# Performance work log

Hardware: AMD Instinct MI355X
Metric: run time of the kernel (lower is better)

Reference implementation:

```python
import jax, jax.numpy as jnp
import numpy as np

V, E, T, H, L, FF = 32000, 512, 2048, 8, 6, 2048
B = 2
HD = E // H
EPS = 1e-5


def setup_inputs() -> dict:
    key = jax.random.key(0)
    ks = iter(jax.random.split(key, 32))
    s = 0.02
    d = {
        "x": jax.random.randint(next(ks), (B, T), 0, V),
        "tok_emb": jax.random.normal(next(ks), (V, E), jnp.float32) * s,
        "pos_emb": jax.random.normal(next(ks), (T, E), jnp.float32) * s,
        "Wq": jax.random.normal(next(ks), (L, E, E), jnp.float32) * s,
        "bq": jnp.zeros((L, E), jnp.float32),
        "Wk": jax.random.normal(next(ks), (L, E, E), jnp.float32) * s,
        "bk": jnp.zeros((L, E), jnp.float32),
        "Wv": jax.random.normal(next(ks), (L, E, E), jnp.float32) * s,
        "bv": jnp.zeros((L, E), jnp.float32),
        "Wo": jax.random.normal(next(ks), (L, E, E), jnp.float32) * s,
        "bo": jnp.zeros((L, E), jnp.float32),
        "ln1_s": jnp.ones((L, E), jnp.float32),
        "ln1_b": jnp.zeros((L, E), jnp.float32),
        "ln2_s": jnp.ones((L, E), jnp.float32),
        "ln2_b": jnp.zeros((L, E), jnp.float32),
        "W1": jax.random.normal(next(ks), (L, E, FF), jnp.float32) * s,
        "b1": jnp.zeros((L, FF), jnp.float32),
        "W2": jax.random.normal(next(ks), (L, FF, E), jnp.float32) * s,
        "b2": jnp.zeros((L, E), jnp.float32),
        "Wout": jax.random.normal(next(ks), (E, V), jnp.float32) * s,
        "bout": jnp.zeros((V,), jnp.float32),
    }
    return d


def _layernorm(x, scale, bias):
    mu = jnp.mean(x, axis=-1, keepdims=True)
    var = jnp.var(x, axis=-1, keepdims=True)
    return (x - mu) * jax.lax.rsqrt(var + EPS) * scale + bias


def reference(x, tok_emb, pos_emb, Wq, bq, Wk, bk, Wv, bv, Wo, bo,
              ln1_s, ln1_b, ln2_s, ln2_b, W1, b1, W2, b2, Wout, bout):
    b, t = x.shape
    h = tok_emb[x] + pos_emb[:t][None]  # [b,t,E]
    causal = jnp.tril(jnp.ones((t, t), bool))  # True on/below diag
    for i in range(L):
        y = _layernorm(h, ln1_s[i], ln1_b[i])
        q = (y @ Wq[i] + bq[i]).reshape(b, t, H, HD)
        k = (y @ Wk[i] + bk[i]).reshape(b, t, H, HD)
        v = (y @ Wv[i] + bv[i]).reshape(b, t, H, HD)
        scores = jnp.einsum("bqhd,bkhd->bhqk", q, k) / np.sqrt(HD).astype(np.float32)
        scores = jnp.where(causal, scores, -jnp.inf)
        attn = jax.nn.softmax(scores, axis=-1)
        o = jnp.einsum("bhqk,bkhd->bqhd", attn, v).reshape(b, t, E)
        h = h + (o @ Wo[i] + bo[i])  # dropout is identity at eval
        y = _layernorm(h, ln2_s[i], ln2_b[i])
        ff = jax.nn.relu(y @ W1[i] + b1[i]) @ W2[i] + b2[i]
        h = h + ff
    return h @ Wout + bout  # [b,t,V]
```

## Files before the change

kernel.cpp:

```cpp
#include <hip/hip_runtime.h>
#include <cstdint>
#include <cstddef>

#define TOKENS 4096
#define E_ 512
#define T_ 2048
#define H_ 8
#define L_ 6
#define FF_ 2048
#define V_ 32000

typedef unsigned short u16;
typedef __attribute__((ext_vector_type(8))) short short8;
typedef __attribute__((ext_vector_type(4))) float f32x4;

__device__ __forceinline__ u16 f2b(float f) {
  union { float f; unsigned u; } x; x.f = f;
  unsigned r = x.u + 0x7fffu + ((x.u >> 16) & 1u);
  return (u16)(r >> 16);
}

__device__ __forceinline__ void gload_lds16(const void* g, void* l) {
  __builtin_amdgcn_global_load_lds((__attribute__((address_space(1))) void*)(uintptr_t)g,
                                   (__attribute__((address_space(3))) void*)l, 16, 0, 0);
}

template<int BF16OUT, int RESID, int RELU>
__global__ __launch_bounds__(256) void gemm_bt(
    const u16* __restrict__ A, const u16* __restrict__ BT,
    const float* __restrict__ bias, const float* __restrict__ resid,
    void* __restrict__ outp, int M, int N, int K, int ldc)
{
  __shared__ u16 a_sm[2][128 * 32];
  __shared__ u16 b_sm[2][128 * 32];
  const int tid  = threadIdx.x;
  const int wave = tid >> 6;
  const int lane = tid & 63;
  const int l16  = lane & 15;
  const int quad = lane >> 4;
  const int bm = blockIdx.y << 7;
  const int bn = blockIdx.x << 7;
  const int wr = (wave >> 1) << 6;
  const int wc = (wave & 1) << 6;

  const int srow = tid >> 2;
  const int soff = (tid & 3) << 3;
  const u16* ag0 = A  + (size_t)(bm + srow) * K + soff;
  const u16* ag1 = A  + (size_t)(bm + 64 + srow) * K + soff;
  const u16* bg0 = BT + (size_t)(bn + srow) * K + soff;
  const u16* bg1 = BT + (size_t)(bn + 64 + srow) * K + soff;

  auto stage = [&](int buf, int k0) {
    gload_lds16(ag0 + k0, a_sm[buf] + wave * 512);
    gload_lds16(ag1 + k0, a_sm[buf] + 2048 + wave * 512);
    gload_lds16(bg0 + k0, b_sm[buf] + wave * 512);
    gload_lds16(bg1 + k0, b_sm[buf] + 2048 + wave * 512);
  };

  f32x4 acc[4][4] = {};
  const int ksteps = K >> 5;
  stage(0, 0);
  int cur = 0;
  for (int t = 0; t < ksteps; ++t) {
    __syncthreads();
    if (t + 1 < ksteps) stage(cur ^ 1, (t + 1) << 5);
    short8 af[4], bf[4];
#pragma unroll
    for (int mt = 0; mt < 4; ++mt)
      af[mt] = *(const short8*)&a_sm[cur][(wr + mt * 16 + l16) * 32 + quad * 8];
#pragma unroll
    for (int nt = 0; nt < 4; ++nt)
      bf[nt] = *(const short8*)&b_sm[cur][(wc + nt * 16 + l16) * 32 + quad * 8];
#pragma unroll
    for (int mt = 0; mt < 4; ++mt)
#pragma unroll
      for (int nt = 0; nt < 4; ++nt)
        acc[mt][nt] = __builtin_amdgcn_mfma_f32_16x16x32_bf16(af[mt], bf[nt], acc[mt][nt], 0, 0, 0);
    cur ^= 1;
  }

#pragma unroll
  for (int mt = 0; mt < 4; ++mt) {
#pragma unroll
    for (int nt = 0; nt < 4; ++nt) {
      const int cg = bn + wc + nt * 16 + l16;
      const int rg = bm + wr + mt * 16 + quad * 4;
      const float bv = bias[cg];
#pragma unroll
      for (int i = 0; i < 4; ++i) {
        float v = acc[mt][nt][i] + bv;
        size_t idx = (size_t)(rg + i) * ldc + cg;
        if (RESID) v += resid[idx];
        if (RELU)  v = fmaxf(v, 0.f);
        if (BF16OUT) ((u16*)outp)[idx] = f2b(v);
        else         ((float*)outp)[idx] = v;
      }
    }
  }
}

template<int BF16OUT, int RELU>
__global__ __launch_bounds__(256) void gemm_bt64(
    const u16* __restrict__ A, const u16* __restrict__ BT,
    const float* __restrict__ bias, void* __restrict__ outp,
    int M, int N, int K, int ldc)
{
  __shared__ u16 a_sm[2][64 * 32];
  __shared__ u16 b_sm[2][128 * 32];
  const int tid  = threadIdx.x;
  const int wave = tid >> 6;
  const int lane = tid & 63;
  const int l16  = lane & 15;
  const int quad = lane >> 4;
  const int bm = blockIdx.y << 6;
  const int bn = blockIdx.x << 7;
  const int wr = (wave >> 1) << 5;
  const int wc = (wave & 1) << 6;

  const int srow = tid >> 2;
  const int soff = (tid & 3) << 3;
  const u16* ag  = A  + (size_t)(bm + srow) * K + soff;
  const u16* bg0 = BT + (size_t)(bn + srow) * K + soff;
  const u16* bg1 = BT + (size_t)(bn + 64 + srow) * K + soff;

  auto stage = [&](int buf, int k0) {
    gload_lds16(ag  + k0, a_sm[buf] + wave * 512);
    gload_lds16(bg0 + k0, b_sm[buf] + wave * 512);
    gload_lds16(bg1 + k0, b_sm[buf] + 2048 + wave * 512);
  };

  f32x4 acc[2][4] = {};
  const int ksteps = K >> 5;
  stage(0, 0);
  int cur = 0;
  for (int t = 0; t < ksteps; ++t) {
    __syncthreads();
    if (t + 1 < ksteps) stage(cur ^ 1, (t + 1) << 5);
    short8 af[2], bf[4];
#pragma unroll
    for (int mt = 0; mt < 2; ++mt)
      af[mt] = *(const short8*)&a_sm[cur][(wr + mt * 16 + l16) * 32 + quad * 8];
#pragma unroll
    for (int nt = 0; nt < 4; ++nt)
      bf[nt] = *(const short8*)&b_sm[cur][(wc + nt * 16 + l16) * 32 + quad * 8];
#pragma unroll
    for (int mt = 0; mt < 2; ++mt)
#pragma unroll
      for (int nt = 0; nt < 4; ++nt)
        acc[mt][nt] = __builtin_amdgcn_mfma_f32_16x16x32_bf16(af[mt], bf[nt], acc[mt][nt], 0, 0, 0);
    cur ^= 1;
  }

#pragma unroll
  for (int mt = 0; mt < 2; ++mt) {
#pragma unroll
    for (int nt = 0; nt < 4; ++nt) {
      const int cg = bn + wc + nt * 16 + l16;
      const int rg = bm + wr + mt * 16 + quad * 4;
      const float bv = bias[cg];
#pragma unroll
      for (int i = 0; i < 4; ++i) {
        float v = acc[mt][nt][i] + bv;
        size_t idx = (size_t)(rg + i) * ldc + cg;
        if (RELU)  v = fmaxf(v, 0.f);
        if (BF16OUT) ((u16*)outp)[idx] = f2b(v);
        else         ((float*)outp)[idx] = v;
      }
    }
  }
}

__global__ __launch_bounds__(256) void gemm_sk64(
    const u16* __restrict__ A, const u16* __restrict__ BT,
    float* __restrict__ part, int M, int N, int lda, int kLen)
{
  __shared__ u16 a_sm[2][64 * 32];
  __shared__ u16 b_sm[2][128 * 32];
  const int tid  = threadIdx.x;
  const int wave = tid >> 6;
  const int lane = tid & 63;
  const int l16  = lane & 15;
  const int quad = lane >> 4;
  const int bm = blockIdx.y << 6;
  const int bn = blockIdx.x << 7;
  const int wr = (wave >> 1) << 5;
  const int wc = (wave & 1) << 6;

  const u16* Ab = A  + (size_t)blockIdx.z * kLen;
  const u16* Bb = BT + (size_t)blockIdx.z * kLen;

  const int srow = tid >> 2;
  const int soff = (tid & 3) << 3;
  const u16* ag  = Ab + (size_t)(bm + srow) * lda + soff;
  const u16* bg0 = Bb + (size_t)(bn + srow) * lda + soff;
  const u16* bg1 = Bb + (size_t)(bn + 64 + srow) * lda + soff;

  auto stage = [&](int buf, int k0) {
    gload_lds16(ag  + k0, a_sm[buf] + wave * 512);
    gload_lds16(bg0 + k0, b_sm[buf] + wave * 512);
    gload_lds16(bg1 + k0, b_sm[buf] + 2048 + wave * 512);
  };

  f32x4 acc[2][4] = {};
  const int ksteps = kLen >> 5;
  stage(0, 0);
  int cur = 0;
  for (int t = 0; t < ksteps; ++t) {
    __syncthreads();
    if (t + 1 < ksteps) stage(cur ^ 1, (t + 1) << 5);
    short8 af[2], bf[4];
#pragma unroll
    for (int mt = 0; mt < 2; ++mt)
      af[mt] = *(const short8*)&a_sm[cur][(wr + mt * 16 + l16) * 32 + quad * 8];
#pragma unroll
    for (int nt = 0; nt < 4; ++nt)
      bf[nt] = *(const short8*)&b_sm[cur][(wc + nt * 16 + l16) * 32 + quad * 8];
#pragma unroll
    for (int mt = 0; mt < 2; ++mt)
#pragma unroll
      for (int nt = 0; nt < 4; ++nt)
        acc[mt][nt] = __builtin_amdgcn_mfma_f32_16x16x32_bf16(af[mt], bf[nt], acc[mt][nt], 0, 0, 0);
    cur ^= 1;
  }

  float* out = part + (size_t)blockIdx.z * M * N;
#pragma unroll
  for (int mt = 0; mt < 2; ++mt) {
#pragma unroll
    for (int nt = 0; nt < 4; ++nt) {
      const int cg = bn + wc + nt * 16 + l16;
      const int rg = bm + wr + mt * 16 + quad * 4;
#pragma unroll
      for (int i = 0; i < 4; ++i)
        out[(size_t)(rg + i) * N + cg] = acc[mt][nt][i];
    }
  }
}

__global__ __launch_bounds__(256) void attn_kernel(const u16* __restrict__ qkv,
                                                   u16* __restrict__ o)
{
  __shared__ u16 k_sm[2][64 * 64];
  __shared__ u16 vT_sm[2][64 * 64];
  __shared__ u16 p_sm[4 * 16 * 64];
  const int tid  = threadIdx.x;
  const int wave = tid >> 6;
  const int lane = tid & 63;
  const int l16  = lane & 15;
  const int quad = lane >> 4;
  const int j  = blockIdx.x;
  const int bh = blockIdx.y;
  const int b  = bh >> 3, h = bh & 7;
  const size_t base = (size_t)b * T_ * 1536;

  const int qrow = j * 64 + wave * 16 + l16;
  short8 aq[2];
#pragma unroll
  for (int half = 0; half < 2; ++half)
    aq[half] = *(const short8*)&qkv[base + (size_t)qrow * 1536 + h * 64 + half * 32 + quad * 8];

  f32x4 oacc[4] = {};
  float m_i[4] = {-INFINITY, -INFINITY, -INFINITY, -INFINITY};
  float l_i[4] = {0.f, 0.f, 0.f, 0.f};

  const int ksrc = ((tid & 7) ^ ((tid >> 3) & 7)) * 8;
  auto stageK = [&](int kt, int buf) {
    gload_lds16(qkv + base + (size_t)(kt * 64 + (tid >> 3)) * 1536 + 512 + h * 64 + ksrc,
                k_sm[buf] + wave * 512);
    gload_lds16(qkv + base + (size_t)(kt * 64 + 32 + (tid >> 3)) * 1536 + 512 + h * 64 + ksrc,
                k_sm[buf] + 2048 + wave * 512);
  };
  const int vt = tid >> 2, vd0 = (tid & 3) * 16;
  auto loadV = [&](int kt, short8* vr) {
    const u16* vp = &qkv[base + (size_t)(kt * 64 + vt) * 1536 + 1024 + h * 64 + vd0];
    vr[0] = *(const short8*)vp;
    vr[1] = *(const short8*)(vp + 8);
  };
  auto writeV = [&](int buf, const short8* vr) {
#pragma unroll
    for (int i = 0; i < 8; ++i) vT_sm[buf][(vd0 + i) * 64 + (vt ^ (i << 3))] = (u16)vr[0][i];
#pragma unroll
    for (int i = 0; i < 8; ++i) vT_sm[buf][(vd0 + 8 + i) * 64 + (vt ^ (i << 3))] = (u16)vr[1][i];
  };

  const int nkt = j + 1;
  short8 vr[2], vrn[2];
  stageK(0, 0);
  loadV(0, vr);
  writeV(0, vr);
  int cur = 0;
  for (int kt = 0; kt < nkt; ++kt) {
    __syncthreads();
    if (kt + 1 < nkt) { stageK(kt + 1, cur ^ 1); loadV(kt + 1, vrn); }

    f32x4 s[4] = {};
#pragma unroll
    for (int nt = 0; nt < 4; ++nt)
#pragma unroll
      for (int half = 0; half < 2; ++half) {
        short8 bk = *(const short8*)&k_sm[cur][(nt * 16 + l16) * 64 +
                                              (((half * 4 + quad) ^ (l16 & 7)) << 3)];
        s[nt] = __builtin_amdgcn_mfma_f32_16x16x32_bf16(aq[half], bk, s[nt], 0, 0, 0);
      }
#pragma unroll
    for (int nt = 0; nt < 4; ++nt)
#pragma unroll
      for (int i = 0; i < 4; ++i) {
        const int col = kt * 64 + nt * 16 + l16;
        const int row = j * 64 + wave * 16 + quad * 4 + i;
        float sv = s[nt][i] * 0.125f;
        s[nt][i] = (col <= row) ? sv : -INFINITY;
      }
    float rm[4], mn[4], alpha[4], rs[4], p[4][4];
#pragma unroll
    for (int i = 0; i < 4; ++i)
      rm[i] = fmaxf(fmaxf(s[0][i], s[1][i]), fmaxf(s[2][i], s[3][i]));
#pragma unroll
    for (int off = 1; off < 16; off <<= 1)
#pragma unroll
      for (int i = 0; i < 4; ++i) rm[i] = fmaxf(rm[i], __shfl_xor(rm[i], off));
#pragma unroll
    for (int i = 0; i < 4; ++i) {
      mn[i] = fmaxf(m_i[i], rm[i]);
      alpha[i] = __expf(m_i[i] - mn[i]);
      m_i[i] = mn[i];
#pragma unroll
      for (int nt = 0; nt < 4; ++nt) p[nt][i] = __expf(s[nt][i] - mn[i]);
      rs[i] = (p[0][i] + p[1][i]) + (p[2][i] + p[3][i]);
    }
#pragma unroll
    for (int off = 1; off < 16; off <<= 1)
#pragma unroll
      for (int i = 0; i < 4; ++i) rs[i] += __shfl_xor(rs[i], off);
#pragma unroll
    for (int i = 0; i < 4; ++i) l_i[i] = l_i[i] * alpha[i] + rs[i];
#pragma unroll
    for (int nt = 0; nt < 4; ++nt)
#pragma unroll
      for (int i = 0; i < 4; ++i) oacc[nt][i] *= alpha[i];
    u16* pw = p_sm + wave * 1024;
#pragma unroll
    for (int i = 0; i < 4; ++i) {
      const int pr = quad * 4 + i;
#pragma unroll
      for (int nt = 0; nt < 4; ++nt)
        pw[pr * 64 + ((nt * 16 + l16) ^ ((pr & 7) << 3))] = f2b(p[nt][i]);
    }
    asm volatile("s_waitcnt lgkmcnt(0)" ::: "memory");
    short8 pf[2];
#pragma unroll
    for (int kh = 0; kh < 2; ++kh)
      pf[kh] = *(const short8*)&pw[l16 * 64 + (((kh * 4 + quad) ^ (l16 & 7)) << 3)];
#pragma unroll
    for (int nt = 0; nt < 4; ++nt)
#pragma unroll
      for (int kh = 0; kh < 2; ++kh) {
        short8 bv = *(const short8*)&vT_sm[cur][(nt * 16 + l16) * 64 +
                                               (((kh * 4 + quad) ^ (l16 & 7)) << 3)];
        oacc[nt] = __builtin_amdgcn_mfma_f32_16x16x32_bf16(pf[kh], bv, oacc[nt], 0, 0, 0);
      }

    if (kt + 1 < nkt) writeV(cur ^ 1, vrn);
    cur ^= 1;
  }
#pragma unroll
  for (int nt = 0; nt < 4; ++nt)
#pragma unroll
    for (int i = 0; i < 4; ++i) {
      const int row = j * 64 + wave * 16 + quad * 4 + i;
      const float ov = oacc[nt][i] / l_i[i];
      o[(size_t)(b * T_ + row) * 512 + h * 64 + nt * 16 + l16] = f2b(ov);
    }
}

__device__ __forceinline__ void ln_emit(float2 hv, const float* __restrict__ sc,
                                        const float* __restrict__ bi, int tid,
                                        unsigned* __restrict__ yrow)
{
  float s = hv.x + hv.y;
  float q = hv.x * hv.x + hv.y * hv.y;
  for (int off = 32; off; off >>= 1) { s += __shfl_down(s, off); q += __shfl_down(q, off); }
  __shared__ float red[8];
  const int wave = tid >> 6, lane = tid & 63;
  if (!lane) { red[wave] = s; red[4 + wave] = q; }
  __syncthreads();
  if (tid == 0) {
    float ts = 0, tq = 0;
    for (int w = 0; w < 4; ++w) { ts += red[w]; tq += red[4 + w]; }
    red[0] = ts; red[4] = tq;
  }
  __syncthreads();
  const float mu = red[0] * (1.f / 512.f);
  const float var = red[4] * (1.f / 512.f) - mu * mu;
  const float rstd = rsqrtf(var + 1e-5f);
  const float y0 = (hv.x - mu) * rstd * sc[tid * 2]     + bi[tid * 2];
  const float y1 = (hv.y - mu) * rstd * sc[tid * 2 + 1] + bi[tid * 2 + 1];
  yrow[tid] = ((unsigned)f2b(y1) << 16) | (unsigned)f2b(y0);
}

template<int NS, int DOLN>
__global__ __launch_bounds__(256) void resid_ln_kernel(
    const float* __restrict__ part, const float* __restrict__ bias,
    float* __restrict__ h, const float* __restrict__ sc,
    const float* __restrict__ bi, u16* __restrict__ y)
{
  const int row = blockIdx.x, tid = threadIdx.x;
  float2 hv = ((const float2*)(h + (size_t)row * 512))[tid];
  const float2 bv = ((const float2*)bias)[tid];
#pragma unroll
  for (int s = 0; s < NS; ++s) {
    const float2 pv = ((const float2*)(part + ((size_t)s * TOKENS + row) * 512))[tid];
    hv.x += pv.x; hv.y += pv.y;
  }
  hv.x += bv.x; hv.y += bv.y;
  ((float2*)(h + (size_t)row * 512))[tid] = hv;
  if (DOLN)
    ln_emit(hv, sc, bi, tid, (unsigned*)(y + (size_t)row * 512));
  else
    ((unsigned*)y)[(size_t)row * 256 + tid] = ((unsigned)f2b(hv.y) << 16) | (unsigned)f2b(hv.x);
}

__global__ __launch_bounds__(256) void embed_ln_kernel(const int* __restrict__ x,
                                                       const float* __restrict__ tok,
                                                       const float* __restrict__ pos,
                                                       const float* __restrict__ sc,
                                                       const float* __restrict__ bi,
                                                       float* __restrict__ h,
                                                       u16* __restrict__ y)
{
  const int row = blockIdx.x, tid = threadIdx.x;
  const int t = row & (T_ - 1);
  const int tk = x[row];
  const float2 a = ((const float2*)tok)[(size_t)tk * 256 + tid];
  const float2 p = ((const float2*)pos)[(size_t)t * 256 + tid];
  float2 hv = make_float2(a.x + p.x, a.y + p.y);
  ((float2*)(h + (size_t)row * 512))[tid] = hv;
  ln_emit(hv, sc, bi, tid, (unsigned*)(y + (size_t)row * 512));
}

__global__ void transW(const float* __restrict__ src, u16* __restrict__ dst,
                       int K, int N, long sStr, long dStr)
{
  __shared__ float tile[32][33];
  const int l = blockIdx.z;
  const float* S = src + (size_t)l * sStr;
  u16* D = dst + (size_t)l * dStr;
  const int n0 = blockIdx.x * 32, k0 = blockIdx.y * 32;
  const int tx = threadIdx.x, ty = threadIdx.y;
#pragma unroll
  for (int i = 0; i < 4; ++i)
    tile[ty + 8 * i][tx] = S[(size_t)(k0 + ty + 8 * i) * N + n0 + tx];
  __syncthreads();
#pragma unroll
  for (int i = 0; i < 4; ++i)
    D[(size_t)(n0 + ty + 8 * i) * K + k0 + tx] = f2b(tile[tx][ty + 8 * i]);
}

__global__ __launch_bounds__(256) void bias_cat_kernel(const float* __restrict__ bq,
                                                       const float* __restrict__ bk,
                                                       const float* __restrict__ bv,
                                                       float* __restrict__ o)
{
  const int i = blockIdx.x * 256 + threadIdx.x;
  if (i >= L_ * 1536) return;
  const int l = i / 1536, c = i % 1536;
  float v = (c < 512) ? bq[l * 512 + c] : (c < 1024) ? bk[l * 512 + c - 512] : bv[l * 512 + c - 1024];
  o[i] = v;
}

extern "C" void kernel_launch(void* const* d_in, const int* in_sizes, int n_in,
                              void* d_out, int out_size, void* d_ws, size_t ws_size,
                              hipStream_t stream) {
  const int*   x     = (const int*)d_in[0];
  const float* tok   = (const float*)d_in[1];
  const float* pos   = (const float*)d_in[2];
  const float* Wq    = (const float*)d_in[3];
  const float* bq    = (const float*)d_in[4];
  const float* Wk    = (const float*)d_in[5];
  const float* bk    = (const float*)d_in[6];
  const float* Wv    = (const float*)d_in[7];
  const float* bv    = (const float*)d_in[8];
  const float* Wo    = (const float*)d_in[9];
  const float* bo    = (const float*)d_in[10];
  const float* ln1s  = (const float*)d_in[11];
  const float* ln1b  = (const float*)d_in[12];
  const float* ln2s  = (const float*)d_in[13];
  const float* ln2b  = (const float*)d_in[14];
  const float* W1    = (const float*)d_in[15];
  const float* b1    = (const float*)d_in[16];
  const float* W2    = (const float*)d_in[17];
  const float* b2    = (const float*)d_in[18];
  const float* Wout  = (const float*)d_in[19];
  const float* bout  = (const float*)d_in[20];

  char* ws = (char*)d_ws;
  size_t off = 0;
  auto alloc = [&](size_t bytes) { char* p = ws + off; off += (bytes + 255) & ~(size_t)255; return p; };
  u16*   qkvT  = (u16*)alloc((size_t)L_ * 1536 * 512 * 2);
  u16*   WoT   = (u16*)alloc((size_t)L_ * 512 * 512 * 2);
  u16*   W1T   = (u16*)alloc((size_t)L_ * 2048 * 512 * 2);
  u16*   W2T   = (u16*)alloc((size_t)L_ * 512 * 2048 * 2);
  u16*   WoutT = (u16*)alloc((size_t)V_ * 512 * 2);
  float* bqkv  = (float*)alloc((size_t)L_ * 1536 * 4);
  float* h     = (float*)alloc((size_t)TOKENS * 512 * 4);
  u16*   y     = (u16*)alloc((size_t)TOKENS * 512 * 2);
  u16*   qkv   = (u16*)alloc((size_t)TOKENS * 1536 * 2);
  u16*   obuf  = (u16*)alloc((size_t)TOKENS * 512 * 2);
  u16*   ff    = (u16*)alloc((size_t)TOKENS * 2048 * 2);
  u16*   hb    = (u16*)alloc((size_t)TOKENS * 512 * 2);
  float* part  = (float*)alloc((size_t)4 * TOKENS * 512 * 4);
  (void)ws_size; (void)in_sizes; (void)n_in; (void)out_size;

  transW<<<dim3(16, 16, L_), dim3(32, 8), 0, stream>>>(Wq, qkvT,             512, 512, 512L * 512, 1536L * 512);
  transW<<<dim3(16, 16, L_), dim3(32, 8), 0, stream>>>(Wk, qkvT + 512 * 512, 512, 512, 512L * 512, 1536L * 512);
  transW<<<dim3(16, 16, L_), dim3(32, 8), 0, stream>>>(Wv, qkvT + 1024 * 512,512, 512, 512L * 512, 1536L * 512);
  transW<<<dim3(16, 16, L_), dim3(32, 8), 0, stream>>>(Wo, WoT,              512, 512, 512L * 512, 512L * 512);
  transW<<<dim3(64, 16, L_), dim3(32, 8), 0, stream>>>(W1, W1T,  512, 2048, 512L * 2048, 2048L * 512);
  transW<<<dim3(16, 64, L_), dim3(32, 8), 0, stream>>>(W2, W2T, 2048,  512, 2048L * 512, 512L * 2048);
  transW<<<dim3(1000, 16, 1), dim3(32, 8), 0, stream>>>(Wout, WoutT, 512, V_, 0, 0);
  bias_cat_kernel<<<36, 256, 0, stream>>>(bq, bk, bv, bqkv);

  embed_ln_kernel<<<TOKENS, 256, 0, stream>>>(x, tok, pos, ln1s, ln1b, h, y);

  for (int l = 0; l < L_; ++l) {
    gemm_bt64<1, 0><<<dim3(12, 64), 256, 0, stream>>>(
        y, qkvT + (size_t)l * 1536 * 512, bqkv + l * 1536, qkv, TOKENS, 1536, 512, 1536);
    attn_kernel<<<dim3(32, 16), 256, 0, stream>>>(qkv, obuf);
    gemm_sk64<<<dim3(4, 64, 2), 256, 0, stream>>>(
        obuf, WoT + (size_t)l * 512 * 512, part, TOKENS, 512, 512, 256);
    resid_ln_kernel<2, 1><<<TOKENS, 256, 0, stream>>>(
        part, bo + l * 512, h, ln2s + l * 512, ln2b + l * 512, y);
    gemm_bt64<1, 1><<<dim3(16, 64), 256, 0, stream>>>(
        y, W1T + (size_t)l * 2048 * 512, b1 + l * 2048, ff, TOKENS, 2048, 512, 2048);
    gemm_sk64<<<dim3(4, 64, 2), 256, 0, stream>>>(
        ff, W2T + (size_t)l * 512 * 2048, part, TOKENS, 512, 2048, 1024);
    if (l < L_ - 1)
      resid_ln_kernel<2, 1><<<TOKENS, 256, 0, stream>>>(
          part, b2 + l * 512, h, ln1s + (l + 1) * 512, ln1b + (l + 1) * 512, y);
    else
      resid_ln_kernel<2, 0><<<TOKENS, 256, 0, stream>>>(
          part, b2 + l * 512, h, nullptr, nullptr, hb);
  }

  gemm_bt<0, 0, 0><<<dim3(250, 32), 256, 0, stream>>>(
      hb, WoutT, bout, nullptr, (float*)d_out, TOKENS, V_, 512, V_);
}
```

Before: 1.833 ms.

## Merge weight-transpose launches, fold bias concat into embed, swizzle and stream logits GEMM

All weight transposes now run in one launch that picks its matrix from the block index, and the QKV bias concat moves into the embedding kernel, removing eight small launches. The vocabulary GEMM remaps block indices across eight groups to change which tiles run together, and writes its fp32 logits with nontemporal stores so they bypass the cache. Attention reverses the query-tile order for the second batch, which is meant to spread causal work more evenly. The split-K partial buffer is shrunk to the two slices actually used, and the unused residual path is removed.

```diff
diff --git a/kernel.cpp b/kernel.cpp
--- a/kernel.cpp
+++ b/kernel.cpp
@@ -25,11 +25,11 @@
                                    (__attribute__((address_space(3))) void*)l, 16, 0, 0);
 }
 
-template<int BF16OUT, int RESID, int RELU>
+template<int BF16OUT, int RELU>
 __global__ __launch_bounds__(256) void gemm_bt(
     const u16* __restrict__ A, const u16* __restrict__ BT,
-    const float* __restrict__ bias, const float* __restrict__ resid,
-    void* __restrict__ outp, int M, int N, int K, int ldc)
+    const float* __restrict__ bias, void* __restrict__ outp,
+    int M, int N, int K, int ldc)
 {
   __shared__ u16 a_sm[2][128 * 32];
   __shared__ u16 b_sm[2][128 * 32];
@@ -38,8 +38,11 @@
   const int lane = tid & 63;
   const int l16  = lane & 15;
   const int quad = lane >> 4;
-  const int bm = blockIdx.y << 7;
-  const int bn = blockIdx.x << 7;
+  int id = blockIdx.y * gridDim.x + blockIdx.x;
+  const int cpx = (gridDim.x * gridDim.y) >> 3;
+  id = (id & 7) * cpx + (id >> 3);
+  const int bm = (id / gridDim.x) << 7;
+  const int bn = (id % gridDim.x) << 7;
   const int wr = (wave >> 1) << 6;
   const int wc = (wave & 1) << 6;
 
@@ -90,10 +93,9 @@
       for (int i = 0; i < 4; ++i) {
         float v = acc[mt][nt][i] + bv;
         size_t idx = (size_t)(rg + i) * ldc + cg;
-        if (RESID) v += resid[idx];
         if (RELU)  v = fmaxf(v, 0.f);
         if (BF16OUT) ((u16*)outp)[idx] = f2b(v);
-        else         ((float*)outp)[idx] = v;
+        else         __builtin_nontemporal_store(v, (float*)outp + idx);
       }
     }
   }
@@ -248,8 +250,8 @@
   const int lane = tid & 63;
   const int l16  = lane & 15;
   const int quad = lane >> 4;
-  const int j  = blockIdx.x;
   const int bh = blockIdx.y;
+  const int j  = (bh < 8) ? blockIdx.x : 31 - blockIdx.x;
   const int b  = bh >> 3, h = bh & 7;
   const size_t base = (size_t)b * T_ * 1536;
 
@@ -425,10 +427,22 @@
                                                        const float* __restrict__ pos,
                                                        const float* __restrict__ sc,
                                                        const float* __restrict__ bi,
+                                                       const float* __restrict__ bq,
+                                                       const float* __restrict__ bk,
+                                                       const float* __restrict__ bv,
+                                                       float* __restrict__ bqkv,
                                                        float* __restrict__ h,
                                                        u16* __restrict__ y)
 {
   const int row = blockIdx.x, tid = threadIdx.x;
+  if (row < 36) {
+    const int i = row * 256 + tid;
+    if (i < L_ * 1536) {
+      const int l = i / 1536, c = i % 1536;
+      bqkv[i] = (c < 512) ? bq[l * 512 + c]
+              : (c < 1024) ? bk[l * 512 + c - 512] : bv[l * 512 + c - 1024];
+    }
+  }
   const int t = row & (T_ - 1);
   const int tk = x[row];
   const float2 a = ((const float2*)tok)[(size_t)tk * 256 + tid];
@@ -438,14 +452,42 @@
   ln_emit(hv, sc, bi, tid, (unsigned*)(y + (size_t)row * 512));
 }
 
-__global__ void transW(const float* __restrict__ src, u16* __restrict__ dst,
-                       int K, int N, long sStr, long dStr)
+__global__ void transW_all(const float* __restrict__ Wq, const float* __restrict__ Wk,
+                           const float* __restrict__ Wv, const float* __restrict__ Wo,
+                           const float* __restrict__ W1, const float* __restrict__ W2,
+                           const float* __restrict__ Wout,
+                           u16* __restrict__ qkvT, u16* __restrict__ WoT,
+                           u16* __restrict__ W1T, u16* __restrict__ W2T,
+                           u16* __restrict__ WoutT)
 {
   __shared__ float tile[32][33];
-  const int l = blockIdx.z;
-  const float* S = src + (size_t)l * sStr;
-  u16* D = dst + (size_t)l * dStr;
-  const int n0 = blockIdx.x * 32, k0 = blockIdx.y * 32;
+  int f = blockIdx.x;
+  const float* S; u16* D; int N, Kd, n0, k0;
+  if (f < 16000) {
+    S = Wout; D = WoutT; N = 32000; Kd = 512;
+    n0 = (f % 1000) * 32; k0 = (f / 1000) * 32;
+  } else {
+    f -= 16000;
+    const int l = f / 3072, r = f % 3072;
+    if (r < 1024) {
+      const int w = r >> 8, rr = r & 255;
+      S = (w == 0 ? Wq : w == 1 ? Wk : w == 2 ? Wv : Wo) + (size_t)l * 512 * 512;
+      D = (w < 3) ? qkvT + (size_t)l * 1536 * 512 + (size_t)w * 512 * 512
+                  : WoT + (size_t)l * 512 * 512;
+      N = 512; Kd = 512;
+      n0 = (rr & 15) * 32; k0 = (rr >> 4) * 32;
+    } else if (r < 2048) {
+      const int rr = r - 1024;
+      S = W1 + (size_t)l * 512 * 2048; D = W1T + (size_t)l * 2048 * 512;
+      N = 2048; Kd = 512;
+      n0 = (rr & 63) * 32; k0 = (rr >> 6) * 32;
+    } else {
+      const int rr = r - 2048;
+      S = W2 + (size_t)l * 2048 * 512; D = W2T + (size_t)l * 512 * 2048;
+      N = 512; Kd = 2048;
+      n0 = (rr & 15) * 32; k0 = (rr >> 4) * 32;
+    }
+  }
   const int tx = threadIdx.x, ty = threadIdx.y;
 #pragma unroll
   for (int i = 0; i < 4; ++i)
@@ -453,19 +495,7 @@
   __syncthreads();
 #pragma unroll
   for (int i = 0; i < 4; ++i)
-    D[(size_t)(n0 + ty + 8 * i) * K + k0 + tx] = f2b(tile[tx][ty + 8 * i]);
-}
-
-__global__ __launch_bounds__(256) void bias_cat_kernel(const float* __restrict__ bq,
-                                                       const float* __restrict__ bk,
-                                                       const float* __restrict__ bv,
-                                                       float* __restrict__ o)
-{
-  const int i = blockIdx.x * 256 + threadIdx.x;
-  if (i >= L_ * 1536) return;
-  const int l = i / 1536, c = i % 1536;
-  float v = (c < 512) ? bq[l * 512 + c] : (c < 1024) ? bk[l * 512 + c - 512] : bv[l * 512 + c - 1024];
-  o[i] = v;
+    D[(size_t)(n0 + ty + 8 * i) * Kd + k0 + tx] = f2b(tile[tx][ty + 8 * i]);
 }
 
 extern "C" void kernel_launch(void* const* d_in, const int* in_sizes, int n_in,
@@ -508,19 +538,14 @@
   u16*   obuf  = (u16*)alloc((size_t)TOKENS * 512 * 2);
   u16*   ff    = (u16*)alloc((size_t)TOKENS * 2048 * 2);
   u16*   hb    = (u16*)alloc((size_t)TOKENS * 512 * 2);
-  float* part  = (float*)alloc((size_t)4 * TOKENS * 512 * 4);
+  float* part  = (float*)alloc((size_t)2 * TOKENS * 512 * 4);
   (void)ws_size; (void)in_sizes; (void)n_in; (void)out_size;
 
-  transW<<<dim3(16, 16, L_), dim3(32, 8), 0, stream>>>(Wq, qkvT,             512, 512, 512L * 512, 1536L * 512);
-  transW<<<dim3(16, 16, L_), dim3(32, 8), 0, stream>>>(Wk, qkvT + 512 * 512, 512, 512, 512L * 512, 1536L * 512);
-  transW<<<dim3(16, 16, L_), dim3(32, 8), 0, stream>>>(Wv, qkvT + 1024 * 512,512, 512, 512L * 512, 1536L * 512);
-  transW<<<dim3(16, 16, L_), dim3(32, 8), 0, stream>>>(Wo, WoT,              512, 512, 512L * 512, 512L * 512);
-  transW<<<dim3(64, 16, L_), dim3(32, 8), 0, stream>>>(W1, W1T,  512, 2048, 512L * 2048, 2048L * 512);
-  transW<<<dim3(16, 64, L_), dim3(32, 8), 0, stream>>>(W2, W2T, 2048,  512, 2048L * 512, 512L * 2048);
-  transW<<<dim3(1000, 16, 1), dim3(32, 8), 0, stream>>>(Wout, WoutT, 512, V_, 0, 0);
-  bias_cat_kernel<<<36, 256, 0, stream>>>(bq, bk, bv, bqkv);
-
-  embed_ln_kernel<<<TOKENS, 256, 0, stream>>>(x, tok, pos, ln1s, ln1b, h, y);
+  transW_all<<<34432, dim3(32, 8), 0, stream>>>(Wq, Wk, Wv, Wo, W1, W2, Wout,
+                                                qkvT, WoT, W1T, W2T, WoutT);
+
+  embed_ln_kernel<<<TOKENS, 256, 0, stream>>>(x, tok, pos, ln1s, ln1b,
+                                              bq, bk, bv, bqkv, h, y);
 
   for (int l = 0; l < L_; ++l) {
     gemm_bt64<1, 0><<<dim3(12, 64), 256, 0, stream>>>(
@@ -542,6 +567,6 @@
           part, b2 + l * 512, h, nullptr, nullptr, hb);
   }
 
-  gemm_bt<0, 0, 0><<<dim3(250, 32), 256, 0, stream>>>(
-      hb, WoutT, bout, nullptr, (float*)d_out, TOKENS, V_, 512, V_);
-}
+  gemm_bt<0, 0><<<dim3(250, 32), 256, 0, stream>>>(
+      hb, WoutT, bout, (float*)d_out, TOKENS, V_, 512, V_);
+}
```

Result: faster. 1.730 ms (-5.6%).
